# Kernel optimization log

Measured on AMD Instinct MI355X. Metric: run time of the kernel, lower is better.

The kernel has to match this reference:

```python
import jax, jax.numpy as jnp
import numpy as np

THRESHOLD = 400.0  # 20*20
ALPHA = 0.1
BETA = 0.9

B, V, J = 16384, 8, 64


def setup_inputs() -> dict:
    key = jax.random.key(0)
    k1, k2, k3, k4, k5 = jax.random.split(key, 5)
    kps_world_gt = jax.random.normal(k1, (B, J, 3), jnp.float32)
    kps_world_pred = kps_world_gt + 0.05 * jax.random.normal(k2, (B, J, 3), jnp.float32)
    eye = jnp.eye(3, dtype=jnp.float32)
    # near-identity "rotations" (orthogonality not needed for the loss math)
    gt_R = eye + 0.05 * jax.random.normal(k3, (B, V, 3, 3), jnp.float32)
    # translations with camera pushed back along +z so depth stays positive
    gt_t = 0.1 * jax.random.normal(k4, (B, V, 3), jnp.float32) + jnp.array([0.0, 0.0, 5.0], jnp.float32)
    # intrinsics: fx=fy=1000, cx=cy=500 per view
    K = jnp.broadcast_to(jnp.array([[1000.0, 0.0, 500.0], [0.0, 1000.0, 500.0], [0.0, 0.0, 1.0]], jnp.float32), (V, 3, 3))
    # predicted [3,4] extrinsics, noisy around gt [R|t]
    E_gt = jnp.concatenate([gt_R, gt_t[..., None]], axis=-1)  # [B,V,3,4]
    cam_preds = E_gt + 0.01 * jax.random.normal(k5, (B, V, 3, 4), jnp.float32)
    return {"kps_world_gt": kps_world_gt, "kps_world_pred": kps_world_pred,
            "gt_R": gt_R, "gt_t": gt_t, "K": K, "cam_preds": cam_preds}


def _smooth_mse(pred, gt):
    # KeypointsMSESmoothLoss per batch element: diff=(gt-pred)^2, threshold reweight, sum/dim
    diff = (gt - pred) ** 2  # [B,V,J,2]
    mask = diff > THRESHOLD
    diff_safe = jnp.where(mask, diff, 1.0)
    big = jnp.power(diff_safe, ALPHA) * (THRESHOLD ** BETA)
    diff = jnp.where(mask, big, diff)
    dim = pred.shape[-1]  # 2
    return jnp.sum(diff, axis=(1, 2, 3)) / dim  # [B]


def reference(kps_world_gt, kps_world_pred, gt_R, gt_t, K, cam_preds):
    # GT projection: x = K @ (R @ X + t), perspective divide
    Xc = jnp.einsum('bvij,bkj->bvki', gt_R, kps_world_gt) + gt_t[:, :, None, :]  # [B,V,J,3]
    x = jnp.einsum('vij,bvkj->bvki', K, Xc)
    gt_proj = x[..., :2] / x[..., 2:3]  # [B,V,J,2]
    # predicted projection via predicted [3,4] camera matrices
    Xh = jnp.concatenate([kps_world_pred, jnp.ones_like(kps_world_pred[..., :1])], axis=-1)  # [B,J,4]
    Xcp = jnp.einsum('bvij,bkj->bvki', cam_preds, Xh)  # [B,V,J,3]
    xp = jnp.einsum('vij,bvkj->bvki', K, Xcp)
    pred_proj = xp[..., :2] / xp[..., 2:3]
    per_batch = _smooth_mse(pred_proj, gt_proj)  # [B]
    return jnp.mean(per_batch)
```

## Files before the change

kernel.cpp:

```cpp
#include <hip/hip_runtime.h>

#define VV 8
#define JJ 64
#define THR 400.0f
#define ALPHA 0.1f

__global__ __launch_bounds__(256) void fold_kernel(
    const float* __restrict__ gt_R,
    const float* __restrict__ gt_t,
    const float* __restrict__ Kmat,
    const float* __restrict__ cam,
    float4* __restrict__ MN,
    int nrows)
{
    const int row = blockIdx.x * 256 + threadIdx.x;
    if (row >= nrows) return;
    const int r = row % 3;
    const int which = (row / 3) & 1;
    const int bv = row / 6;
    const int v = bv & (VV - 1);

    const float* Kv = Kmat + v * 9 + r * 3;
    const float k0 = Kv[0], k1 = Kv[1], k2 = Kv[2];

    float4 o;
    if (which == 0) {
        const float* R = gt_R + (size_t)bv * 9;
        const float* t = gt_t + (size_t)bv * 3;
        o.x = fmaf(k0, R[0], fmaf(k1, R[3], k2 * R[6]));
        o.y = fmaf(k0, R[1], fmaf(k1, R[4], k2 * R[7]));
        o.z = fmaf(k0, R[2], fmaf(k1, R[5], k2 * R[8]));
        o.w = fmaf(k0, t[0], fmaf(k1, t[1], k2 * t[2]));
    } else {
        const float4* C = (const float4*)(cam + (size_t)bv * 12);
        const float4 c0 = C[0], c1 = C[1], c2 = C[2];
        o.x = fmaf(k0, c0.x, fmaf(k1, c1.x, k2 * c2.x));
        o.y = fmaf(k0, c0.y, fmaf(k1, c1.y, k2 * c2.y));
        o.z = fmaf(k0, c0.z, fmaf(k1, c1.z, k2 * c2.z));
        o.w = fmaf(k0, c0.w, fmaf(k1, c1.w, k2 * c2.w));
    }
    MN[row] = o;
}

__global__ __launch_bounds__(256) void loss_kernel(
    const float* __restrict__ kps_gt,
    const float* __restrict__ kps_pred,
    const float4* __restrict__ MN,
    float* __restrict__ partials)
{
    __shared__ float s_red[4];
    const int tid = threadIdx.x;
    const int lane = tid & 63;
    const int wave = tid >> 6;
    const int b = __builtin_amdgcn_readfirstlane(blockIdx.x * 4 + wave);

    const float* g = kps_gt + (size_t)b * (JJ * 3) + lane * 3;
    const float X0 = g[0], X1 = g[1], X2 = g[2];
    const float* p = kps_pred + (size_t)b * (JJ * 3) + lane * 3;
    const float P0 = p[0], P1 = p[1], P2 = p[2];

    const float4* mn = MN + (size_t)b * (VV * 6);
    const float c09 = powf(THR, 0.9f);

    float acc = 0.0f;
#pragma unroll
    for (int v = 0; v < VV; ++v) {
        const float4 M0 = mn[v * 6 + 0];
        const float4 M1 = mn[v * 6 + 1];
        const float4 M2 = mn[v * 6 + 2];
        const float4 N0 = mn[v * 6 + 3];
        const float4 N1 = mn[v * 6 + 4];
        const float4 N2 = mn[v * 6 + 5];

        const float x0 = fmaf(M0.x, X0, fmaf(M0.y, X1, fmaf(M0.z, X2, M0.w)));
        const float x1 = fmaf(M1.x, X0, fmaf(M1.y, X1, fmaf(M1.z, X2, M1.w)));
        const float x2 = fmaf(M2.x, X0, fmaf(M2.y, X1, fmaf(M2.z, X2, M2.w)));
        const float rg = __builtin_amdgcn_rcpf(x2);
        const float g0 = x0 * rg;
        const float g1 = x1 * rg;

        const float y0 = fmaf(N0.x, P0, fmaf(N0.y, P1, fmaf(N0.z, P2, N0.w)));
        const float y1 = fmaf(N1.x, P0, fmaf(N1.y, P1, fmaf(N1.z, P2, N1.w)));
        const float y2 = fmaf(N2.x, P0, fmaf(N2.y, P1, fmaf(N2.z, P2, N2.w)));
        const float rp = __builtin_amdgcn_rcpf(y2);
        const float q0 = y0 * rp;
        const float q1 = y1 * rp;

        float d0 = g0 - q0; d0 *= d0;
        float d1 = g1 - q1; d1 *= d1;
        if (d0 > THR) d0 = __builtin_amdgcn_exp2f(ALPHA * __builtin_amdgcn_logf(d0)) * c09;
        if (d1 > THR) d1 = __builtin_amdgcn_exp2f(ALPHA * __builtin_amdgcn_logf(d1)) * c09;
        acc += d0 + d1;
    }

#pragma unroll
    for (int off = 32; off > 0; off >>= 1)
        acc += __shfl_down(acc, off, 64);

    if (lane == 0) s_red[wave] = acc;
    __syncthreads();
    if (tid == 0)
        partials[blockIdx.x] = s_red[0] + s_red[1] + s_red[2] + s_red[3];
}

__global__ __launch_bounds__(256) void reduce_kernel(
    const float* __restrict__ partials, float* __restrict__ out,
    float scale, int n)
{
    __shared__ float s_red[4];
    const int tid = threadIdx.x;
    float acc = 0.0f;
    for (int i = tid; i < n; i += 256)
        acc += partials[i];
#pragma unroll
    for (int off = 32; off > 0; off >>= 1)
        acc += __shfl_down(acc, off, 64);
    const int wave = tid >> 6;
    const int lane = tid & 63;
    if (lane == 0) s_red[wave] = acc;
    __syncthreads();
    if (tid == 0)
        out[0] = (s_red[0] + s_red[1] + s_red[2] + s_red[3]) * scale;
}

extern "C" void kernel_launch(void* const* d_in, const int* in_sizes, int n_in,
                              void* d_out, int out_size, void* d_ws, size_t ws_size,
                              hipStream_t stream) {
    const float* kps_gt   = (const float*)d_in[0];
    const float* kps_pred = (const float*)d_in[1];
    const float* gt_R     = (const float*)d_in[2];
    const float* gt_t     = (const float*)d_in[3];
    const float* Kmat     = (const float*)d_in[4];
    const float* cam      = (const float*)d_in[5];
    float* out = (float*)d_out;

    const int B = in_sizes[0] / (JJ * 3);
    const float scale = 1.0f / (2.0f * (float)B);

    float4* MN = (float4*)d_ws;
    float* partials = (float*)((char*)d_ws + (size_t)B * VV * 6 * sizeof(float4));

    const int nrows = B * VV * 6;
    fold_kernel<<<(nrows + 255) / 256, 256, 0, stream>>>(gt_R, gt_t, Kmat, cam,
                                                         MN, nrows);
    loss_kernel<<<B / 4, 256, 0, stream>>>(kps_gt, kps_pred, MN, partials);
    reduce_kernel<<<1, 256, 0, stream>>>(partials, out, scale, B / 4);
}
```

Baseline: 105.2 us.

## Fuse camera-matrix folding into loss kernel via per-wave LDS staging

```diff
diff --git a/kernel.cpp b/kernel.cpp
--- a/kernel.cpp
+++ b/kernel.cpp
@@ -4,114 +4,139 @@
 #define JJ 64
 #define THR 400.0f
 #define ALPHA 0.1f
+#define NB 2048
+#define BITER 2
 
-__global__ __launch_bounds__(256) void fold_kernel(
+__global__ __launch_bounds__(256) void proj_loss_kernel(
+    const float* __restrict__ kps_gt,
+    const float* __restrict__ kps_pred,
     const float* __restrict__ gt_R,
     const float* __restrict__ gt_t,
     const float* __restrict__ Kmat,
     const float* __restrict__ cam,
-    float4* __restrict__ MN,
-    int nrows)
-{
-    const int row = blockIdx.x * 256 + threadIdx.x;
-    if (row >= nrows) return;
-    const int r = row % 3;
-    const int which = (row / 3) & 1;
-    const int bv = row / 6;
-    const int v = bv & (VV - 1);
-
-    const float* Kv = Kmat + v * 9 + r * 3;
-    const float k0 = Kv[0], k1 = Kv[1], k2 = Kv[2];
-
-    float4 o;
-    if (which == 0) {
-        const float* R = gt_R + (size_t)bv * 9;
-        const float* t = gt_t + (size_t)bv * 3;
-        o.x = fmaf(k0, R[0], fmaf(k1, R[3], k2 * R[6]));
-        o.y = fmaf(k0, R[1], fmaf(k1, R[4], k2 * R[7]));
-        o.z = fmaf(k0, R[2], fmaf(k1, R[5], k2 * R[8]));
-        o.w = fmaf(k0, t[0], fmaf(k1, t[1], k2 * t[2]));
-    } else {
-        const float4* C = (const float4*)(cam + (size_t)bv * 12);
-        const float4 c0 = C[0], c1 = C[1], c2 = C[2];
-        o.x = fmaf(k0, c0.x, fmaf(k1, c1.x, k2 * c2.x));
-        o.y = fmaf(k0, c0.y, fmaf(k1, c1.y, k2 * c2.y));
-        o.z = fmaf(k0, c0.z, fmaf(k1, c1.z, k2 * c2.z));
-        o.w = fmaf(k0, c0.w, fmaf(k1, c1.w, k2 * c2.w));
-    }
-    MN[row] = o;
-}
-
-__global__ __launch_bounds__(256) void loss_kernel(
-    const float* __restrict__ kps_gt,
-    const float* __restrict__ kps_pred,
-    const float4* __restrict__ MN,
     float* __restrict__ partials)
 {
-    __shared__ float s_red[4];
-    const int tid = threadIdx.x;
+    __shared__ float  s_K[VV * 9];
+    __shared__ float  s_stage[4][192];
+    __shared__ float4 s_MN[4][48];
+    __shared__ float  s_red[4];
+
+    const int tid  = threadIdx.x;
     const int lane = tid & 63;
-    const int wave = tid >> 6;
-    const int b = __builtin_amdgcn_readfirstlane(blockIdx.x * 4 + wave);
+    const int w    = tid >> 6;
 
-    const float* g = kps_gt + (size_t)b * (JJ * 3) + lane * 3;
-    const float X0 = g[0], X1 = g[1], X2 = g[2];
-    const float* p = kps_pred + (size_t)b * (JJ * 3) + lane * 3;
-    const float P0 = p[0], P1 = p[1], P2 = p[2];
+    if (tid < VV * 9) s_K[tid] = Kmat[tid];
+    __syncthreads();
 
-    const float4* mn = MN + (size_t)b * (VV * 6);
+    const int fv    = lane / 6;
+    const int fidx  = lane - fv * 6;
+    const int fwhich = (fidx >= 3) ? 1 : 0;
+    const int fr    = fidx - 3 * fwhich;
+    float k0 = 0.f, k1 = 0.f, k2 = 0.f;
+    if (lane < 48) {
+        k0 = s_K[fv * 9 + fr * 3 + 0];
+        k1 = s_K[fv * 9 + fr * 3 + 1];
+        k2 = s_K[fv * 9 + fr * 3 + 2];
+    }
+
+    float*  stg = s_stage[w];
+    float4* mn  = s_MN[w];
     const float c09 = powf(THR, 0.9f);
 
     float acc = 0.0f;
+
 #pragma unroll
-    for (int v = 0; v < VV; ++v) {
-        const float4 M0 = mn[v * 6 + 0];
-        const float4 M1 = mn[v * 6 + 1];
-        const float4 M2 = mn[v * 6 + 2];
-        const float4 N0 = mn[v * 6 + 3];
-        const float4 N1 = mn[v * 6 + 4];
-        const float4 N2 = mn[v * 6 + 5];
+    for (int it = 0; it < BITER; ++it) {
+        const int b = blockIdx.x * (4 * BITER) + it * 4 + w;
 
-        const float x0 = fmaf(M0.x, X0, fmaf(M0.y, X1, fmaf(M0.z, X2, M0.w)));
-        const float x1 = fmaf(M1.x, X0, fmaf(M1.y, X1, fmaf(M1.z, X2, M1.w)));
-        const float x2 = fmaf(M2.x, X0, fmaf(M2.y, X1, fmaf(M2.z, X2, M2.w)));
-        const float rg = __builtin_amdgcn_rcpf(x2);
-        const float g0 = x0 * rg;
-        const float g1 = x1 * rg;
+        const float* Rb = gt_R + (size_t)b * 72;
+        const float* tb = gt_t + (size_t)b * 24;
+        const float* Cb = cam  + (size_t)b * 96;
+        stg[lane] = Rb[lane];
+        if (lane < 8)  stg[64 + lane] = Rb[64 + lane];
+        if (lane < 24) stg[72 + lane] = tb[lane];
+        stg[96 + lane] = Cb[lane];
+        if (lane < 32) stg[160 + lane] = Cb[64 + lane];
 
-        const float y0 = fmaf(N0.x, P0, fmaf(N0.y, P1, fmaf(N0.z, P2, N0.w)));
-        const float y1 = fmaf(N1.x, P0, fmaf(N1.y, P1, fmaf(N1.z, P2, N1.w)));
-        const float y2 = fmaf(N2.x, P0, fmaf(N2.y, P1, fmaf(N2.z, P2, N2.w)));
-        const float rp = __builtin_amdgcn_rcpf(y2);
-        const float q0 = y0 * rp;
-        const float q1 = y1 * rp;
+        const float* g = kps_gt   + (size_t)b * (JJ * 3) + lane * 3;
+        const float* p = kps_pred + (size_t)b * (JJ * 3) + lane * 3;
+        const float X0 = g[0], X1 = g[1], X2 = g[2];
+        const float P0 = p[0], P1 = p[1], P2 = p[2];
 
-        float d0 = g0 - q0; d0 *= d0;
-        float d1 = g1 - q1; d1 *= d1;
-        if (d0 > THR) d0 = __builtin_amdgcn_exp2f(ALPHA * __builtin_amdgcn_logf(d0)) * c09;
-        if (d1 > THR) d1 = __builtin_amdgcn_exp2f(ALPHA * __builtin_amdgcn_logf(d1)) * c09;
-        acc += d0 + d1;
+        __builtin_amdgcn_wave_barrier();
+
+        if (lane < 48) {
+            float4 o;
+            if (!fwhich) {
+                const float* R = &stg[fv * 9];
+                const float* t = &stg[72 + fv * 3];
+                o.x = fmaf(k0, R[0], fmaf(k1, R[3], k2 * R[6]));
+                o.y = fmaf(k0, R[1], fmaf(k1, R[4], k2 * R[7]));
+                o.z = fmaf(k0, R[2], fmaf(k1, R[5], k2 * R[8]));
+                o.w = fmaf(k0, t[0], fmaf(k1, t[1], k2 * t[2]));
+            } else {
+                const float* C = &stg[96 + fv * 12];
+                o.x = fmaf(k0, C[0], fmaf(k1, C[4], k2 * C[8]));
+                o.y = fmaf(k0, C[1], fmaf(k1, C[5], k2 * C[9]));
+                o.z = fmaf(k0, C[2], fmaf(k1, C[6], k2 * C[10]));
+                o.w = fmaf(k0, C[3], fmaf(k1, C[7], k2 * C[11]));
+            }
+            mn[fv * 6 + fwhich * 3 + fr] = o;
+        }
+
+        __builtin_amdgcn_wave_barrier();
+
+#pragma unroll
+        for (int v = 0; v < VV; ++v) {
+            const float4 M0 = mn[v * 6 + 0];
+            const float4 M1 = mn[v * 6 + 1];
+            const float4 M2 = mn[v * 6 + 2];
+            const float4 N0 = mn[v * 6 + 3];
+            const float4 N1 = mn[v * 6 + 4];
+            const float4 N2 = mn[v * 6 + 5];
+
+            const float x0 = fmaf(M0.x, X0, fmaf(M0.y, X1, fmaf(M0.z, X2, M0.w)));
+            const float x1 = fmaf(M1.x, X0, fmaf(M1.y, X1, fmaf(M1.z, X2, M1.w)));
+            const float x2 = fmaf(M2.x, X0, fmaf(M2.y, X1, fmaf(M2.z, X2, M2.w)));
+            const float rg = __builtin_amdgcn_rcpf(x2);
+            const float g0 = x0 * rg;
+            const float g1 = x1 * rg;
+
+            const float y0 = fmaf(N0.x, P0, fmaf(N0.y, P1, fmaf(N0.z, P2, N0.w)));
+            const float y1 = fmaf(N1.x, P0, fmaf(N1.y, P1, fmaf(N1.z, P2, N1.w)));
+            const float y2 = fmaf(N2.x, P0, fmaf(N2.y, P1, fmaf(N2.z, P2, N2.w)));
+            const float rp = __builtin_amdgcn_rcpf(y2);
+            const float q0 = y0 * rp;
+            const float q1 = y1 * rp;
+
+            float d0 = g0 - q0; d0 *= d0;
+            float d1 = g1 - q1; d1 *= d1;
+            if (d0 > THR) d0 = __builtin_amdgcn_exp2f(ALPHA * __builtin_amdgcn_logf(d0)) * c09;
+            if (d1 > THR) d1 = __builtin_amdgcn_exp2f(ALPHA * __builtin_amdgcn_logf(d1)) * c09;
+            acc += d0 + d1;
+        }
+
+        __builtin_amdgcn_wave_barrier();
     }
 
 #pragma unroll
     for (int off = 32; off > 0; off >>= 1)
         acc += __shfl_down(acc, off, 64);
-
-    if (lane == 0) s_red[wave] = acc;
+    if (lane == 0) s_red[w] = acc;
     __syncthreads();
     if (tid == 0)
         partials[blockIdx.x] = s_red[0] + s_red[1] + s_red[2] + s_red[3];
 }
 
 __global__ __launch_bounds__(256) void reduce_kernel(
-    const float* __restrict__ partials, float* __restrict__ out,
-    float scale, int n)
+    const float* __restrict__ partials, float* __restrict__ out, float scale)
 {
     __shared__ float s_red[4];
     const int tid = threadIdx.x;
     float acc = 0.0f;
-    for (int i = tid; i < n; i += 256)
-        acc += partials[i];
+#pragma unroll
+    for (int i = 0; i < NB / 256; ++i)
+        acc += partials[tid + i * 256];
 #pragma unroll
     for (int off = 32; off > 0; off >>= 1)
         acc += __shfl_down(acc, off, 64);
@@ -133,16 +158,13 @@
     const float* Kmat     = (const float*)d_in[4];
     const float* cam      = (const float*)d_in[5];
     float* out = (float*)d_out;
+    float* partials = (float*)d_ws;
 
     const int B = in_sizes[0] / (JJ * 3);
     const float scale = 1.0f / (2.0f * (float)B);
+    (void)B;
 
-    float4* MN = (float4*)d_ws;
-    float* partials = (float*)((char*)d_ws + (size_t)B * VV * 6 * sizeof(float4));
-
-    const int nrows = B * VV * 6;
-    fold_kernel<<<(nrows + 255) / 256, 256, 0, stream>>>(gt_R, gt_t, Kmat, cam,
-                                                         MN, nrows);
-    loss_kernel<<<B / 4, 256, 0, stream>>>(kps_gt, kps_pred, MN, partials);
-    reduce_kernel<<<1, 256, 0, stream>>>(partials, out, scale, B / 4);
+    proj_loss_kernel<<<NB, 256, 0, stream>>>(kps_gt, kps_pred, gt_R, gt_t,
+                                             Kmat, cam, partials);
+    reduce_kernel<<<1, 256, 0, stream>>>(partials, out, scale);
 }
```

Measured after the change: 107.4 us. 1.02x slower.
